# Kernel tuning notes

Measured on AMD Instinct MI355X. Metric: run time of the kernel, lower is better.

Reference implementation:

```python
import jax, jax.numpy as jnp
import numpy as np

DIM = 768
NUM_HEADS = 12
HEAD_DIM = DIM // NUM_HEADS
SCALE = HEAD_DIM ** (-0.5)
MASK_VAL = -10000000.0


def setup_inputs() -> dict:
    key = jax.random.key(0)
    k1, k2, k3, k4 = jax.random.split(key, 4)
    B, N = 2, 2048
    inputs = jax.random.normal(k1, (B, N, DIM), dtype=jnp.float32)
    padding_mask = jax.random.randint(k2, (B, N), 0, 2, dtype=jnp.int32)
    # Xavier-uniform-ish scaled weights
    w_qkv = jax.random.normal(k3, (3 * DIM, DIM), dtype=jnp.float32) * (1.0 / np.sqrt(DIM))
    w_fc = jax.random.normal(k4, (DIM, DIM), dtype=jnp.float32) * (1.0 / np.sqrt(DIM))
    b_fc = jnp.zeros((DIM,), dtype=jnp.float32)
    return {"inputs": inputs, "padding_mask": padding_mask,
            "w_qkv": w_qkv, "w_fc": w_fc, "b_fc": b_fc}


def reference(inputs, padding_mask, w_qkv, w_fc, b_fc):
    B, N, C = inputs.shape
    # qkv projection (torch Linear: x @ W^T), no bias
    qkv = jnp.einsum('bnc,dc->bnd', inputs, w_qkv)          # [B, N, 3*C]
    qkv = qkv.reshape(B, N, 3, NUM_HEADS, HEAD_DIM)
    qkv = jnp.transpose(qkv, (2, 0, 3, 1, 4))               # [3, B, H, N, hd]
    q, k, v = qkv[0], qkv[1], qkv[2]
    # scores: [B, H, N, N]
    att = jnp.einsum('bhqd,bhkd->bhqk', q, k) * SCALE
    mask = padding_mask[:, None, None, :]                   # [B,1,1,N]
    att = jnp.where(mask > 0, MASK_VAL, att)
    att = jax.nn.softmax(att, axis=-1)
    x = jnp.einsum('bhqk,bhkd->bhqd', att, v)               # [B,H,N,hd]
    x = jnp.transpose(x, (0, 2, 1, 3)).reshape(B, N, C)
    x = jnp.einsum('bnc,dc->bnd', x, w_fc) + b_fc
    return x
```

## Files before the change

### kernel.cpp

```cpp
#include <hip/hip_runtime.h>
#include <hip/hip_bf16.h>

#define DIM_  768
#define NH    12
#define HD    64
#define BB    2
#define NN    2048
#define MM    (BB*NN)
#define QKVD  (3*DIM_)

typedef __attribute__((ext_vector_type(8))) short          bf16x8;
typedef __attribute__((ext_vector_type(4))) float          f32x4;

__device__ __forceinline__ unsigned short f2bf(float f) {
    __hip_bfloat16 h = __float2bfloat16(f);
    unsigned short u; __builtin_memcpy(&u, &h, 2); return u;
}

__device__ __forceinline__ void gload16(const void* g, void* lds) {
    __builtin_amdgcn_global_load_lds(
        (const __attribute__((address_space(1))) void*)g,
        (__attribute__((address_space(3))) void*)lds, 16, 0, 0);
}

__global__ __launch_bounds__(256)
void cast_all(const float* __restrict__ x, const float* __restrict__ wqkv,
              const float* __restrict__ wfc, unsigned short* __restrict__ xb,
              unsigned short* __restrict__ wqkvb, unsigned short* __restrict__ wfcb)
{
    const int NV0 = (MM * DIM_) / 4;
    const int NV1 = NV0 + (QKVD * DIM_) / 4;
    const int NV2 = NV1 + (DIM_ * DIM_) / 4;
    int i = blockIdx.x * 256 + threadIdx.x;
    if (i >= NV2) return;
    const float* src; unsigned short* dst;
    if (i < NV0)      { src = x + (size_t)i * 4;            dst = xb + (size_t)i * 4; }
    else if (i < NV1) { size_t j = i - NV0; src = wqkv + j * 4; dst = wqkvb + j * 4; }
    else              { size_t j = i - NV1; src = wfc + j * 4;  dst = wfcb + j * 4; }
    float4 v = *(const float4*)src;
    ushort4 o; o.x = f2bf(v.x); o.y = f2bf(v.y); o.z = f2bf(v.z); o.w = f2bf(v.w);
    *(ushort4*)dst = o;
}

__global__ __launch_bounds__(256)
void gemm_qkv(const unsigned short* __restrict__ A, const unsigned short* __restrict__ W,
              unsigned short* __restrict__ qh, unsigned short* __restrict__ kh,
              unsigned short* __restrict__ vth)
{
    __shared__ unsigned short As[2][128 * 32];
    __shared__ unsigned short Bs[2][128 * 32];
    const int tid = threadIdx.x, lane = tid & 63, wave = tid >> 6;
    const int wr = wave >> 1, wc = wave & 1;
    const int n0 = blockIdx.x * 128, m0 = blockIdx.y * 128;
    const int ldrow = lane >> 2, ldg = lane & 3;
    constexpr float QSCALE = 0.18033688011112042f;

    f32x4 acc[4][4];
    #pragma unroll
    for (int i = 0; i < 4; ++i)
        #pragma unroll
        for (int j = 0; j < 4; ++j) acc[i][j] = (f32x4){0.f, 0.f, 0.f, 0.f};

    #define STAGE_G(buf, k0)                                                         \
        _Pragma("unroll")                                                            \
        for (int rd = 0; rd < 2; ++rd) {                                             \
            const int chunk = rd * 4 + wave;                                         \
            const int row = chunk * 16 + ldrow;                                      \
            gload16(A + (size_t)(m0 + row) * DIM_ + (k0) + ldg * 8,                  \
                    (char*)As[buf] + chunk * 1024);                                  \
            gload16(W + (size_t)(n0 + row) * DIM_ + (k0) + ldg * 8,                  \
                    (char*)Bs[buf] + chunk * 1024);                                  \
        }

    STAGE_G(0, 0);
    __syncthreads();
    int cur = 0;
    for (int kt = 0; kt < DIM_ / 32; ++kt) {
        if (kt < DIM_ / 32 - 1) { STAGE_G(cur ^ 1, (kt + 1) * 32); }
        bf16x8 af[4], bw[4];
        #pragma unroll
        for (int i = 0; i < 4; ++i)
            af[i] = *(const bf16x8*)((const char*)As[cur] + (wr*64 + i*16 + (lane & 15)) * 64 + (lane >> 4) * 16);
        #pragma unroll
        for (int j = 0; j < 4; ++j)
            bw[j] = *(const bf16x8*)((const char*)Bs[cur] + (wc*64 + j*16 + (lane & 15)) * 64 + (lane >> 4) * 16);
        #pragma unroll
        for (int i = 0; i < 4; ++i)
            #pragma unroll
            for (int j = 0; j < 4; ++j)
                acc[i][j] = __builtin_amdgcn_mfma_f32_16x16x32_bf16(af[i], bw[j], acc[i][j], 0, 0, 0);
        __syncthreads();
        cur ^= 1;
    }

    const int r0 = (lane >> 4) * 4, cl = lane & 15;
    const int s = n0 / DIM_;
    const int rem0 = n0 - s * DIM_ + wc * 64;
    if (s == 2) {
        #pragma unroll
        for (int j = 0; j < 4; ++j) {
            const int rem = rem0 + j * 16 + cl;
            const int hh = rem >> 6, dd = rem & 63;
            #pragma unroll
            for (int i = 0; i < 4; ++i) {
                const int mb = m0 + wr * 64 + i * 16 + r0;
                const int bq = mb >> 11, nq0 = mb & 2047;
                const size_t hb = (size_t)(bq * NH + hh);
                ushort4 v;
                v.x = f2bf(acc[i][j][0]); v.y = f2bf(acc[i][j][1]);
                v.z = f2bf(acc[i][j][2]); v.w = f2bf(acc[i][j][3]);
                *(ushort4*)(vth + (hb * 64 + dd) * NN + nq0) = v;
            }
        }
    } else {
        unsigned short* const dstb = (s == 0) ? qh : kh;
        const float sc = (s == 0) ? QSCALE : 1.0f;
        #pragma unroll
        for (int j = 0; j < 4; ++j) {
            const int rem = rem0 + j * 16 + cl;
            const int hh = rem >> 6, dd = rem & 63;
            #pragma unroll
            for (int i = 0; i < 4; ++i) {
                const int mb = m0 + wr * 64 + i * 16 + r0;
                const int bq = mb >> 11, nq0 = mb & 2047;
                const size_t hb = (size_t)(bq * NH + hh);
                unsigned short* dst = dstb + (hb * NN + nq0) * 64 + dd;
                #pragma unroll
                for (int r = 0; r < 4; ++r) dst[(size_t)r * 64] = f2bf(acc[i][j][r] * sc);
            }
        }
    }
    #undef STAGE_G
}

__global__ __launch_bounds__(256)
void gemm_fc(const unsigned short* __restrict__ A, const unsigned short* __restrict__ W,
             const float* __restrict__ bias, float* __restrict__ C, int Md, int Nd, int K)
{
    __shared__ unsigned short As[2][128 * 32];
    __shared__ unsigned short Bs[2][64 * 32];
    const int tid = threadIdx.x, lane = tid & 63, wave = tid >> 6;
    const int wr = wave >> 1, wc = wave & 1;
    const int n0 = blockIdx.x * 64, m0 = blockIdx.y * 128;
    const int ldrow = lane >> 2, ldg = lane & 3;

    f32x4 acc[4][2];
    #pragma unroll
    for (int i = 0; i < 4; ++i)
        #pragma unroll
        for (int j = 0; j < 2; ++j) acc[i][j] = (f32x4){0.f, 0.f, 0.f, 0.f};

    #define STAGE_G(buf, k0)                                                         \
        _Pragma("unroll")                                                            \
        for (int rd = 0; rd < 2; ++rd) {                                             \
            const int chunk = rd * 4 + wave;                                         \
            const int row = chunk * 16 + ldrow;                                      \
            gload16(A + (size_t)(m0 + row) * K + (k0) + ldg * 8,                     \
                    (char*)As[buf] + chunk * 1024);                                  \
        }                                                                            \
        gload16(W + (size_t)(n0 + wave * 16 + ldrow) * K + (k0) + ldg * 8,           \
                (char*)Bs[buf] + wave * 1024);

    STAGE_G(0, 0);
    __syncthreads();
    int cur = 0;
    const int nk = K / 32;
    for (int kt = 0; kt < nk; ++kt) {
        if (kt < nk - 1) { STAGE_G(cur ^ 1, (kt + 1) * 32); }
        bf16x8 af[4], bw[2];
        #pragma unroll
        for (int i = 0; i < 4; ++i)
            af[i] = *(const bf16x8*)((const char*)As[cur] + (wr*64 + i*16 + (lane & 15)) * 64 + (lane >> 4) * 16);
        #pragma unroll
        for (int j = 0; j < 2; ++j)
            bw[j] = *(const bf16x8*)((const char*)Bs[cur] + (wc*32 + j*16 + (lane & 15)) * 64 + (lane >> 4) * 16);
        #pragma unroll
        for (int i = 0; i < 4; ++i)
            #pragma unroll
            for (int j = 0; j < 2; ++j)
                acc[i][j] = __builtin_amdgcn_mfma_f32_16x16x32_bf16(af[i], bw[j], acc[i][j], 0, 0, 0);
        __syncthreads();
        cur ^= 1;
    }

    const int r0 = (lane >> 4) * 4, cl = lane & 15;
    #pragma unroll
    for (int i = 0; i < 4; ++i)
        #pragma unroll
        for (int j = 0; j < 2; ++j) {
            const int n = n0 + wc * 32 + j * 16 + cl;
            const float bv = bias[n];
            #pragma unroll
            for (int r = 0; r < 4; ++r) {
                const int m = m0 + wr * 64 + i * 16 + r0 + r;
                C[(size_t)m * Nd + n] = acc[i][j][r] + bv;
            }
        }
    #undef STAGE_G
}

__global__ __launch_bounds__(256)
void attn_mfma(const unsigned short* __restrict__ qh, const unsigned short* __restrict__ kh,
               const unsigned short* __restrict__ vth, const int* __restrict__ pmask,
               unsigned short* __restrict__ xout)
{
    __shared__ unsigned short Qs[64 * 64];
    __shared__ unsigned short Ks[2][64 * 64];
    __shared__ unsigned short Vs[2][64 * 64];
    __shared__ unsigned short Ps[4][16 * 72];
    __shared__ __align__(16) float maskf[2][64];

    const int tid = threadIdx.x, lane = tid & 63, wave = tid >> 6;
    const int g = lane >> 4, q15 = lane & 15, l7 = lane & 7;
    const int swz = (blockIdx.x & 7) * 96 + (blockIdx.x >> 3);
    const int qt = swz & 31;
    const int bh = swz >> 5;
    const int h = bh % NH, b = bh / NH;
    const size_t base = (size_t)(b * NH + h) * NN * 64;

    const int sr = lane >> 3, sg = lane & 7;

    #define STAGE_KV(buf, kt)                                                          \
        _Pragma("unroll")                                                              \
        for (int rd = 0; rd < 2; ++rd) {                                               \
            const int chunk = rd * 4 + wave;                                           \
            const int row = chunk * 8 + sr;                                            \
            const int gs = (sg ^ (sr & 7)) * 8;                                        \
            gload16(kh + base + (size_t)((kt) * 64 + row) * 64 + gs,                   \
                    (char*)Ks[buf] + chunk * 1024);                                    \
            gload16(vth + base + (size_t)row * NN + (kt) * 64 + gs,                    \
                    (char*)Vs[buf] + chunk * 1024);                                    \
        }

    #pragma unroll
    for (int rd = 0; rd < 2; ++rd) {
        const int chunk = rd * 4 + wave;
        const int row = chunk * 8 + sr;
        gload16(qh + base + (size_t)(qt * 64 + row) * 64 + (sg ^ (sr & 7)) * 8,
                (char*)Qs + chunk * 1024);
    }
    STAGE_KV(0, 0);
    if (tid < 64) maskf[0][tid] = (pmask[b * NN + tid] > 0) ? -__builtin_inff() : 0.f;
    __syncthreads();

    bf16x8 qf[2];
    {
        const int qrow = wave * 16 + q15;
        #pragma unroll
        for (int ks = 0; ks < 2; ++ks) {
            const int gq = (g + ks * 4) ^ l7;
            qf[ks] = *(const bf16x8*)((const char*)Qs + qrow * 128 + gq * 16);
        }
    }

    float m = -1e30f, lsum = 0.f;
    f32x4 oacc[4];
    #pragma unroll
    for (int fo = 0; fo < 4; ++fo) oacc[fo] = (f32x4){0.f, 0.f, 0.f, 0.f};

    int cur = 0;
    for (int kt = 0; kt < NN / 64; ++kt) {
        if (kt < NN / 64 - 1) {
            STAGE_KV(cur ^ 1, kt + 1);
            if (tid < 64)
                maskf[cur ^ 1][tid] = (pmask[b * NN + (kt + 1) * 64 + tid] > 0) ? -__builtin_inff() : 0.f;
        }

        f32x4 s[4];
        #pragma unroll
        for (int f = 0; f < 4; ++f) s[f] = *(const f32x4*)&maskf[cur][f * 16 + g * 4];
        __builtin_amdgcn_s_setprio(1);
        #pragma unroll
        for (int ks = 0; ks < 2; ++ks) {
            #pragma unroll
            for (int f = 0; f < 4; ++f) {
                const int krow = f * 16 + q15;
                const int gk = (g + ks * 4) ^ l7;
                bf16x8 kf = *(const bf16x8*)((const char*)Ks[cur] + krow * 128 + gk * 16);
                s[f] = __builtin_amdgcn_mfma_f32_16x16x32_bf16(kf, qf[ks], s[f], 0, 0, 0);
            }
        }
        __builtin_amdgcn_s_setprio(0);

        float pmax;
        {
            const float a0 = fmaxf(fmaxf(s[0][0], s[0][1]), fmaxf(s[0][2], s[0][3]));
            const float a1 = fmaxf(fmaxf(s[1][0], s[1][1]), fmaxf(s[1][2], s[1][3]));
            const float a2 = fmaxf(fmaxf(s[2][0], s[2][1]), fmaxf(s[2][2], s[2][3]));
            const float a3 = fmaxf(fmaxf(s[3][0], s[3][1]), fmaxf(s[3][2], s[3][3]));
            pmax = fmaxf(fmaxf(a0, a1), fmaxf(a2, a3));
        }
        pmax = fmaxf(pmax, __shfl_xor(pmax, 16));
        pmax = fmaxf(pmax, __shfl_xor(pmax, 32));
        if (__any(pmax > m + 10.0f)) {
            const float mnew = fmaxf(m, pmax);
            const float corr = __builtin_amdgcn_exp2f(m - mnew);
            m = mnew;
            lsum *= corr;
            float c[4];
            #pragma unroll
            for (int r = 0; r < 4; ++r) c[r] = __shfl(corr, g * 4 + r);
            #pragma unroll
            for (int fo = 0; fo < 4; ++fo)
                #pragma unroll
                for (int r = 0; r < 4; ++r) oacc[fo][r] *= c[r];
        }
        float pw[4][4], ps = 0.f;
        #pragma unroll
        for (int f = 0; f < 4; ++f)
            #pragma unroll
            for (int r = 0; r < 4; ++r) {
                const float p = __builtin_amdgcn_exp2f(s[f][r] - m);
                pw[f][r] = p; ps += p;
            }
        ps += __shfl_xor(ps, 16);
        ps += __shfl_xor(ps, 32);
        lsum += ps;

        unsigned short* pb = &Ps[wave][0];
        #pragma unroll
        for (int f = 0; f < 4; ++f) {
            ushort4 u;
            u.x = f2bf(pw[f][0]); u.y = f2bf(pw[f][1]);
            u.z = f2bf(pw[f][2]); u.w = f2bf(pw[f][3]);
            *(ushort4*)(pb + q15 * 72 + f * 16 + g * 4) = u;
        }

        __builtin_amdgcn_s_setprio(1);
        #pragma unroll
        for (int ks = 0; ks < 2; ++ks) {
            bf16x8 pf = *(const bf16x8*)((const char*)pb + (q15 * 72 + ks * 32 + g * 8) * 2);
            #pragma unroll
            for (int fo = 0; fo < 4; ++fo) {
                const int gv = (g + ks * 4) ^ l7;
                bf16x8 vf = *(const bf16x8*)((const char*)Vs[cur] + (fo * 16 + q15) * 128 + gv * 16);
                oacc[fo] = __builtin_amdgcn_mfma_f32_16x16x32_bf16(pf, vf, oacc[fo], 0, 0, 0);
            }
        }
        __builtin_amdgcn_s_setprio(0);

        __syncthreads();
        cur ^= 1;
    }

    float linv[4];
    #pragma unroll
    for (int r = 0; r < 4; ++r) linv[r] = 1.0f / __shfl(lsum, g * 4 + r);
    #pragma unroll
    for (int r = 0; r < 4; ++r) {
        const int q = qt * 64 + wave * 16 + g * 4 + r;
        #pragma unroll
        for (int fo = 0; fo < 4; ++fo) {
            const int d = fo * 16 + q15;
            xout[(size_t)(b * NN + q) * DIM_ + h * 64 + d] = f2bf(oacc[fo][r] * linv[r]);
        }
    }
    #undef STAGE_KV
}

extern "C" void kernel_launch(void* const* d_in, const int* in_sizes, int n_in,
                              void* d_out, int out_size, void* d_ws, size_t ws_size,
                              hipStream_t stream)
{
    const float* x     = (const float*)d_in[0];
    const int*   pmask = (const int*)d_in[1];
    const float* wqkv  = (const float*)d_in[2];
    const float* wfc   = (const float*)d_in[3];
    const float* bfc   = (const float*)d_in[4];
    float* out = (float*)d_out;

    const size_t n_x    = (size_t)MM * DIM_;
    const size_t n_wqkv = (size_t)QKVD * DIM_;
    const size_t n_wfc  = (size_t)DIM_ * DIM_;
    const size_t n_head = (size_t)BB * NH * NN * 64;

    unsigned short* xb    = (unsigned short*)d_ws;
    unsigned short* wqkvb = xb + n_x;
    unsigned short* wfcb  = wqkvb + n_wqkv;
    unsigned short* qhb   = wfcb + n_wfc;
    unsigned short* khb   = qhb + n_head;
    unsigned short* vthb  = khb + n_head;
    unsigned short* xattb = vthb + n_head;

    const int nv = (int)((n_x + n_wqkv + n_wfc) / 4);
    cast_all<<<(nv + 255) / 256, 256, 0, stream>>>(x, wqkv, wfc, xb, wqkvb, wfcb);

    gemm_qkv<<<dim3(QKVD / 128, MM / 128), 256, 0, stream>>>(xb, wqkvb, qhb, khb, vthb);
    attn_mfma<<<dim3(BB * NH * (NN / 64)), 256, 0, stream>>>(qhb, khb, vthb, pmask, xattb);
    gemm_fc<<<dim3(DIM_ / 64, MM / 128), 256, 0, stream>>>(xattb, wfcb, bfc, out, MM, DIM_, DIM_);
}
```

Baseline: 179.8 us.

## Stage QKV epilogue through LDS and shuffle P in registers in attention

The QKV GEMM epilogue now writes its accumulators into a swizzled LDS pool and then emits coalesced 16-byte global stores for Q, K and the transposed V, replacing scattered 2-byte and 8-byte stores. The attention kernel loads Q fragments straight from global memory and precomputes the whole padding mask for the batch row into LDS once, instead of staging 64 mask values per tile. It also converts P to bf16 with packed cvt instructions and rearranges it via cross-lane shuffles rather than a round trip through LDS. This cuts LDS traffic and global store inefficiency, at the cost of extra shuffles and a larger LDS mask buffer.

```diff
diff --git a/kernel.cpp b/kernel.cpp
--- a/kernel.cpp
+++ b/kernel.cpp
@@ -15,6 +15,12 @@
 __device__ __forceinline__ unsigned short f2bf(float f) {
     __hip_bfloat16 h = __float2bfloat16(f);
     unsigned short u; __builtin_memcpy(&u, &h, 2); return u;
+}
+
+__device__ __forceinline__ unsigned int cvt_pk_bf16(float lo, float hi) {
+    unsigned int r;
+    asm("v_cvt_pk_bf16_f32 %0, %1, %2" : "=v"(r) : "v"(lo), "v"(hi));
+    return r;
 }
 
 __device__ __forceinline__ void gload16(const void* g, void* lds) {
@@ -47,12 +53,13 @@
               unsigned short* __restrict__ qh, unsigned short* __restrict__ kh,
               unsigned short* __restrict__ vth)
 {
-    __shared__ unsigned short As[2][128 * 32];
-    __shared__ unsigned short Bs[2][128 * 32];
+    __shared__ unsigned short smem[4][4096];
+    unsigned short* const pool = &smem[0][0];
     const int tid = threadIdx.x, lane = tid & 63, wave = tid >> 6;
     const int wr = wave >> 1, wc = wave & 1;
     const int n0 = blockIdx.x * 128, m0 = blockIdx.y * 128;
     const int ldrow = lane >> 2, ldg = lane & 3;
+    const int g = lane >> 4, q15 = lane & 15;
     constexpr float QSCALE = 0.18033688011112042f;
 
     f32x4 acc[4][4];
@@ -67,9 +74,9 @@
             const int chunk = rd * 4 + wave;                                         \
             const int row = chunk * 16 + ldrow;                                      \
             gload16(A + (size_t)(m0 + row) * DIM_ + (k0) + ldg * 8,                  \
-                    (char*)As[buf] + chunk * 1024);                                  \
+                    (char*)&smem[buf][0] + chunk * 1024);                            \
             gload16(W + (size_t)(n0 + row) * DIM_ + (k0) + ldg * 8,                  \
-                    (char*)Bs[buf] + chunk * 1024);                                  \
+                    (char*)&smem[2 + (buf)][0] + chunk * 1024);                      \
         }
 
     STAGE_G(0, 0);
@@ -80,10 +87,10 @@
         bf16x8 af[4], bw[4];
         #pragma unroll
         for (int i = 0; i < 4; ++i)
-            af[i] = *(const bf16x8*)((const char*)As[cur] + (wr*64 + i*16 + (lane & 15)) * 64 + (lane >> 4) * 16);
+            af[i] = *(const bf16x8*)((const char*)&smem[cur][0] + (wr*64 + i*16 + q15) * 64 + g * 16);
         #pragma unroll
         for (int j = 0; j < 4; ++j)
-            bw[j] = *(const bf16x8*)((const char*)Bs[cur] + (wc*64 + j*16 + (lane & 15)) * 64 + (lane >> 4) * 16);
+            bw[j] = *(const bf16x8*)((const char*)&smem[2 + cur][0] + (wc*64 + j*16 + q15) * 64 + g * 16);
         #pragma unroll
         for (int i = 0; i < 4; ++i)
             #pragma unroll
@@ -92,45 +99,68 @@
         __syncthreads();
         cur ^= 1;
     }
-
-    const int r0 = (lane >> 4) * 4, cl = lane & 15;
+    #undef STAGE_G
+
     const int s = n0 / DIM_;
-    const int rem0 = n0 - s * DIM_ + wc * 64;
+    const int bq = m0 >> 11, nq0 = m0 & 2047;
     if (s == 2) {
         #pragma unroll
         for (int j = 0; j < 4; ++j) {
-            const int rem = rem0 + j * 16 + cl;
-            const int hh = rem >> 6, dd = rem & 63;
+            const int col = wc * 64 + j * 16 + q15;
+            const int cs = (col & 7) << 3;
             #pragma unroll
             for (int i = 0; i < 4; ++i) {
-                const int mb = m0 + wr * 64 + i * 16 + r0;
-                const int bq = mb >> 11, nq0 = mb & 2047;
-                const size_t hb = (size_t)(bq * NH + hh);
+                const int row0 = wr * 64 + i * 16 + g * 4;
                 ushort4 v;
                 v.x = f2bf(acc[i][j][0]); v.y = f2bf(acc[i][j][1]);
                 v.z = f2bf(acc[i][j][2]); v.w = f2bf(acc[i][j][3]);
-                *(ushort4*)(vth + (hb * 64 + dd) * NN + nq0) = v;
-            }
+                *(ushort4*)&pool[col * 128 + ((row0 & ~7) ^ cs) + (row0 & 7)] = v;
+            }
+        }
+        __syncthreads();
+        const int hh0 = (n0 - 2 * DIM_) >> 6;
+        #pragma unroll
+        for (int pass = 0; pass < 8; ++pass) {
+            const int idx = pass * 256 + tid;
+            const int t = idx >> 10;
+            const int ddl = (idx & 1023) >> 4;
+            const int tok0 = (idx & 15) << 3;
+            const int col = t * 64 + ddl;
+            const unsigned short* src = &pool[col * 128 + (tok0 ^ ((col & 7) << 3))];
+            unsigned short* dst = vth + ((size_t)((bq * NH + hh0 + t) * 64 + ddl)) * NN + nq0 + tok0;
+            *(ulonglong2*)dst = *(const ulonglong2*)src;
         }
     } else {
+        const float sc = (s == 0) ? QSCALE : 1.0f;
+        #pragma unroll
+        for (int j = 0; j < 4; ++j) {
+            const int colE = wc * 64 + j * 16 + q15;
+            #pragma unroll
+            for (int i = 0; i < 4; ++i) {
+                #pragma unroll
+                for (int r = 0; r < 4; ++r) {
+                    const int row = wr * 64 + i * 16 + g * 4 + r;
+                    pool[row * 128 + (((colE & ~7) ^ ((row & 7) << 3)) | (colE & 7))] =
+                        f2bf(acc[i][j][r] * sc);
+                }
+            }
+        }
+        __syncthreads();
+        const int hh0 = (n0 - s * DIM_) >> 6;
         unsigned short* const dstb = (s == 0) ? qh : kh;
-        const float sc = (s == 0) ? QSCALE : 1.0f;
-        #pragma unroll
-        for (int j = 0; j < 4; ++j) {
-            const int rem = rem0 + j * 16 + cl;
-            const int hh = rem >> 6, dd = rem & 63;
-            #pragma unroll
-            for (int i = 0; i < 4; ++i) {
-                const int mb = m0 + wr * 64 + i * 16 + r0;
-                const int bq = mb >> 11, nq0 = mb & 2047;
-                const size_t hb = (size_t)(bq * NH + hh);
-                unsigned short* dst = dstb + (hb * NN + nq0) * 64 + dd;
-                #pragma unroll
-                for (int r = 0; r < 4; ++r) dst[(size_t)r * 64] = f2bf(acc[i][j][r] * sc);
-            }
-        }
-    }
-    #undef STAGE_G
+        #pragma unroll
+        for (int pass = 0; pass < 8; ++pass) {
+            const int idx = pass * 256 + tid;
+            const int t = idx >> 10;
+            const int off = idx & 1023;
+            const int tok = off >> 3;
+            const int d0 = (off & 7) << 3;
+            const int colb = t * 64 + d0;
+            const unsigned short* src = &pool[tok * 128 + (colb ^ ((tok & 7) << 3))];
+            unsigned short* dst = dstb + ((size_t)((bq * NH + hh0 + t)) * NN + nq0 + tok) * 64 + d0;
+            *(ulonglong2*)dst = *(const ulonglong2*)src;
+        }
+    }
 }
 
 __global__ __launch_bounds__(256)
@@ -204,14 +234,13 @@
                const unsigned short* __restrict__ vth, const int* __restrict__ pmask,
                unsigned short* __restrict__ xout)
 {
-    __shared__ unsigned short Qs[64 * 64];
     __shared__ unsigned short Ks[2][64 * 64];
     __shared__ unsigned short Vs[2][64 * 64];
-    __shared__ unsigned short Ps[4][16 * 72];
-    __shared__ __align__(16) float maskf[2][64];
+    __shared__ __align__(16) float maskLg[NN];
 
     const int tid = threadIdx.x, lane = tid & 63, wave = tid >> 6;
     const int g = lane >> 4, q15 = lane & 15, l7 = lane & 7;
+    const int X = (lane >> 5) & 1, Y = (lane >> 4) & 1;
     const int swz = (blockIdx.x & 7) * 96 + (blockIdx.x >> 3);
     const int qt = swz & 31;
     const int bh = swz >> 5;
@@ -232,26 +261,25 @@
                     (char*)Vs[buf] + chunk * 1024);                                    \
         }
 
-    #pragma unroll
-    for (int rd = 0; rd < 2; ++rd) {
-        const int chunk = rd * 4 + wave;
-        const int row = chunk * 8 + sr;
-        gload16(qh + base + (size_t)(qt * 64 + row) * 64 + (sg ^ (sr & 7)) * 8,
-                (char*)Qs + chunk * 1024);
-    }
     STAGE_KV(0, 0);
-    if (tid < 64) maskf[0][tid] = (pmask[b * NN + tid] > 0) ? -__builtin_inff() : 0.f;
-    __syncthreads();
-
+    #pragma unroll
+    for (int jj = 0; jj < 2; ++jj) {
+        const int j = jj * 256 + tid;
+        int4 mv = ((const int4*)(pmask + b * NN))[j];
+        float4 mf;
+        mf.x = mv.x > 0 ? -__builtin_inff() : 0.f;
+        mf.y = mv.y > 0 ? -__builtin_inff() : 0.f;
+        mf.z = mv.z > 0 ? -__builtin_inff() : 0.f;
+        mf.w = mv.w > 0 ? -__builtin_inff() : 0.f;
+        ((float4*)maskLg)[j] = mf;
+    }
     bf16x8 qf[2];
     {
-        const int qrow = wave * 16 + q15;
-        #pragma unroll
-        for (int ks = 0; ks < 2; ++ks) {
-            const int gq = (g + ks * 4) ^ l7;
-            qf[ks] = *(const bf16x8*)((const char*)Qs + qrow * 128 + gq * 16);
-        }
-    }
+        const unsigned short* qp = qh + base + (size_t)(qt * 64 + wave * 16 + q15) * 64;
+        qf[0] = *(const bf16x8*)(qp + g * 8);
+        qf[1] = *(const bf16x8*)(qp + 32 + g * 8);
+    }
+    __syncthreads();
 
     float m = -1e30f, lsum = 0.f;
     f32x4 oacc[4];
@@ -260,15 +288,11 @@
 
     int cur = 0;
     for (int kt = 0; kt < NN / 64; ++kt) {
-        if (kt < NN / 64 - 1) {
-            STAGE_KV(cur ^ 1, kt + 1);
-            if (tid < 64)
-                maskf[cur ^ 1][tid] = (pmask[b * NN + (kt + 1) * 64 + tid] > 0) ? -__builtin_inff() : 0.f;
-        }
+        if (kt < NN / 64 - 1) { STAGE_KV(cur ^ 1, kt + 1); }
 
         f32x4 s[4];
         #pragma unroll
-        for (int f = 0; f < 4; ++f) s[f] = *(const f32x4*)&maskf[cur][f * 16 + g * 4];
+        for (int f = 0; f < 4; ++f) s[f] = *(const f32x4*)&maskLg[kt * 64 + f * 16 + g * 4];
         __builtin_amdgcn_s_setprio(1);
         #pragma unroll
         for (int ks = 0; ks < 2; ++ks) {
@@ -307,29 +331,37 @@
         }
         float pw[4][4], ps = 0.f;
         #pragma unroll
-        for (int f = 0; f < 4; ++f)
+        for (int f = 0; f < 4; ++f) {
+            float psf = 0.f;
             #pragma unroll
             for (int r = 0; r < 4; ++r) {
                 const float p = __builtin_amdgcn_exp2f(s[f][r] - m);
-                pw[f][r] = p; ps += p;
-            }
+                pw[f][r] = p; psf += p;
+            }
+            ps += psf;
+        }
         ps += __shfl_xor(ps, 16);
         ps += __shfl_xor(ps, 32);
         lsum += ps;
 
-        unsigned short* pb = &Ps[wave][0];
-        #pragma unroll
-        for (int f = 0; f < 4; ++f) {
-            ushort4 u;
-            u.x = f2bf(pw[f][0]); u.y = f2bf(pw[f][1]);
-            u.z = f2bf(pw[f][2]); u.w = f2bf(pw[f][3]);
-            *(ushort4*)(pb + q15 * 72 + f * 16 + g * 4) = u;
-        }
-
         __builtin_amdgcn_s_setprio(1);
         #pragma unroll
         for (int ks = 0; ks < 2; ++ks) {
-            bf16x8 pf = *(const bf16x8*)((const char*)pb + (q15 * 72 + ks * 32 + g * 8) * 2);
+            unsigned int D00 = cvt_pk_bf16(pw[2*ks+0][0], pw[2*ks+0][1]);
+            unsigned int D01 = cvt_pk_bf16(pw[2*ks+0][2], pw[2*ks+0][3]);
+            unsigned int D10 = cvt_pk_bf16(pw[2*ks+1][0], pw[2*ks+1][1]);
+            unsigned int D11 = cvt_pk_bf16(pw[2*ks+1][2], pw[2*ks+1][3]);
+            unsigned int r0 = (unsigned int)__shfl_xor((int)(X ? D00 : D10), 32);
+            unsigned int r1 = (unsigned int)__shfl_xor((int)(X ? D01 : D11), 32);
+            unsigned int E00 = X ? r0 : D00, E01 = X ? r1 : D01;
+            unsigned int E10 = X ? D10 : r0, E11 = X ? D11 : r1;
+            unsigned int u0 = (unsigned int)__shfl_xor((int)(Y ? E00 : E10), 16);
+            unsigned int u1 = (unsigned int)__shfl_xor((int)(Y ? E01 : E11), 16);
+            unsigned int F0 = Y ? u0 : E00, F1 = Y ? u1 : E01;
+            unsigned int F2 = Y ? E10 : u0, F3 = Y ? E11 : u1;
+            unsigned int pfw[4] = {F0, F1, F2, F3};
+            bf16x8 pf;
+            __builtin_memcpy(&pf, pfw, 16);
             #pragma unroll
             for (int fo = 0; fo < 4; ++fo) {
                 const int gv = (g + ks * 4) ^ l7;
```

Measured after the change: 184.4 us. 2.6% more time.
